# Kernel tuning notes

Measured on AMD Instinct MI355X. Metric: run time of the kernel, lower is better.

Reference implementation:

```python
import jax, jax.numpy as jnp
import numpy as np
from jax import lax

P = 4
PSIZE = P * P
ITERS = 3
EPS = 1e-8
LAMBDA = 1e-3  # inverse-temperature used by the EM routing sigmoid (yl-1993 style)
LN2PI_HALF = 0.5 * float(np.log(2.0 * np.pi))


def extract_patches(x, K, stride, pad):
    """x: (b,h,w,c) -> (b,oh,ow,K*K,c) sliding-window patches."""
    if pad:
        x = jnp.pad(x, ((0, 0), (pad, pad), (pad, pad), (0, 0)))
    b, h, w, c = x.shape
    oh = (h - K) // stride + 1
    ow = (w - K) // stride + 1
    slices = []
    for ki in range(K):
        for kj in range(K):
            slices.append(x[:, ki:ki + stride * (oh - 1) + 1:stride,
                             kj:kj + stride * (ow - 1) + 1:stride, :])
    return jnp.stack(slices, axis=3)  # (b,oh,ow,K*K,c)


def em_routing(v, a_in, beta_u, beta_a, iters=ITERS):
    """EM routing (Hinton et al. 2018).
    v: (n, Bin, Cout, PSIZE) votes, a_in: (n, Bin, 1) input activations.
    Returns mu: (n, Cout, PSIZE), a_out: (n, Cout).
    """
    n, Bin, Cout, psize = v.shape
    r = jnp.full((n, Bin, Cout), 1.0 / Cout, dtype=v.dtype)
    mu = None
    a_out = None
    for it in range(iters):
        # ---- M step ----
        r_w = r * a_in                                    # (n,Bin,Cout)
        r_sum = r_w.sum(axis=1, keepdims=True)            # (n,1,Cout)
        coeff = (r_w / (r_sum + EPS))[..., None]          # (n,Bin,Cout,1)
        mu = jnp.sum(coeff * v, axis=1, keepdims=True)    # (n,1,Cout,psize)
        sigma_sq = jnp.sum(coeff * (v - mu) ** 2, axis=1, keepdims=True) + EPS
        cost_h = (beta_u[None, None, :, None] + 0.5 * jnp.log(sigma_sq)) * r_sum[..., None]
        a_out = jax.nn.sigmoid(LAMBDA * (beta_a[None, None, :] - cost_h.sum(axis=3)))  # (n,1,Cout)
        # ---- E step ----
        if it < iters - 1:
            ln_p = -(v - mu) ** 2 / (2.0 * sigma_sq) - 0.5 * jnp.log(sigma_sq) - LN2PI_HALF
            ln_ap = ln_p.sum(axis=3) + jnp.log(EPS + a_out)  # (n,Bin,Cout)
            r = jax.nn.softmax(ln_ap, axis=2)
    return mu[:, 0], a_out[:, 0]


def depthwise_caps(pose, a, W, bu, ba, K, stride):
    """DepthWiseConvCaps: each capsule type routes its own KxK spatial patch to one
    output capsule of the same type. W: (K*K, B, P, P)."""
    b = pose.shape[0]
    Bc = a.shape[-1]
    pad = K // 2
    pp = extract_patches(pose, K, stride, pad)  # (b,oh,ow,KK,B*PSIZE)
    ap = extract_patches(a, K, stride, pad)     # (b,oh,ow,KK,B)
    oh, ow = pp.shape[1], pp.shape[2]
    pm = pp.reshape(b, oh, ow, K * K, Bc, P, P)
    v = jnp.einsum('bhwkcij,kcjl->bhwkcil', pm, W)            # (b,oh,ow,KK,B,P,P)
    v = v.transpose(0, 1, 2, 4, 3, 5, 6).reshape(b * oh * ow * Bc, K * K, 1, PSIZE)
    a_in = ap.transpose(0, 1, 2, 4, 3).reshape(b * oh * ow * Bc, K * K, 1)
    mu, a_out = em_routing(v, a_in, bu, ba)
    return mu.reshape(b, oh, ow, Bc * PSIZE), a_out.reshape(b, oh, ow, Bc)


def conv_caps_1x1(pose, a, W, bu, ba):
    """ConvCaps with K=1, stride=1: per-position routing Bin -> Cout. W: (Bin,Cout,P,P)."""
    b, h, w, _ = pose.shape
    Bc, Cc = W.shape[0], W.shape[1]
    pm = pose.reshape(b * h * w, Bc, P, P)
    v = jnp.einsum('nbij,bcjl->nbcil', pm, W).reshape(b * h * w, Bc, Cc, PSIZE)
    a_in = a.reshape(b * h * w, Bc)[..., None]
    mu, a_out = em_routing(v, a_in, bu, ba)
    return mu.reshape(b, h, w, Cc * PSIZE), a_out.reshape(b, h, w, Cc)


def class_caps(pose, a, W, bu, ba):
    """Class ConvCaps: w_shared across positions + coordinate addition. W: (D,E,P,P)."""
    b, h, w, _ = pose.shape
    D, E = W.shape[0], W.shape[1]
    pm = pose.reshape(b, h, w, D, P, P)
    v = jnp.einsum('bhwdij,dejl->bhwdeil', pm, W).reshape(b, h, w, D, E, PSIZE)
    # coordinate addition on the first two vote components
    coord = jnp.zeros((h, w, PSIZE), v.dtype)
    coord = coord.at[:, :, 0].add(jnp.arange(h, dtype=v.dtype)[:, None] / h)
    coord = coord.at[:, :, 1].add(jnp.arange(w, dtype=v.dtype)[None, :] / w)
    v = v + coord[None, :, :, None, None, :]
    v = v.reshape(b, h * w * D, E, PSIZE)
    a_in = a.reshape(b, h * w * D, 1)
    mu, a_out = em_routing(v, a_in, bu, ba)
    return mu, a_out  # (b,E,PSIZE), (b,E)


def _forward(x, conv1_w, conv1_b, prim_pose_w, prim_pose_b, prim_a_w, prim_a_b,
             dw1_w, dw1_bu, dw1_ba, cc1_w, cc1_bu, cc1_ba,
             dw2_w, dw2_bu, dw2_ba, cc2_w, cc2_bu, cc2_ba,
             cls_w, cls_bu, cls_ba):
    # conv stem: k5 s2 valid
    y = lax.conv_general_dilated(x, conv1_w, (2, 2), 'VALID',
                                 dimension_numbers=('NHWC', 'HWIO', 'NHWC'))
    y = jax.nn.relu(y + conv1_b)
    # primary caps: 1x1 convs for pose and activation
    pose = jnp.einsum('bhwc,cd->bhwd', y, prim_pose_w) + prim_pose_b   # (b,h,w,B*PSIZE)
    a = jax.nn.sigmoid(jnp.einsum('bhwc,cd->bhwd', y, prim_a_w) + prim_a_b)  # (b,h,w,B)
    pose, a = depthwise_caps(pose, a, dw1_w, dw1_bu, dw1_ba, K=7, stride=2)
    pose, a = conv_caps_1x1(pose, a, cc1_w, cc1_bu, cc1_ba)
    pose, a = depthwise_caps(pose, a, dw2_w, dw2_bu, dw2_ba, K=5, stride=2)
    pose, a = conv_caps_1x1(pose, a, cc2_w, cc2_bu, cc2_ba)
    pose_cls, a_cls = class_caps(pose, a, cls_w, cls_bu, cls_ba)
    return a_cls  # (b, E)


def setup_inputs() -> dict:
    key = jax.random.key(0)
    ks = jax.random.split(key, 10)
    f32 = jnp.float32
    d = {}
    d['x'] = jax.random.normal(ks[0], (32, 64, 64, 1), f32)
    d['conv1_w'] = jax.random.normal(ks[1], (5, 5, 1, 64), f32) * 0.1
    d['conv1_b'] = jnp.zeros((64,), f32)
    d['prim_pose_w'] = jax.random.normal(ks[2], (64, 128), f32) * 0.1
    d['prim_pose_b'] = jnp.zeros((128,), f32)
    d['prim_a_w'] = jax.random.normal(ks[3], (64, 8), f32) * 0.1
    d['prim_a_b'] = jnp.zeros((8,), f32)
    d['dw1_w'] = jax.random.normal(ks[4], (49, 8, 4, 4), f32) * 0.25
    d['dw1_bu'] = jnp.zeros((1,), f32)
    d['dw1_ba'] = jnp.zeros((1,), f32)
    d['cc1_w'] = jax.random.normal(ks[5], (8, 16, 4, 4), f32) * 0.25
    d['cc1_bu'] = jnp.zeros((16,), f32)
    d['cc1_ba'] = jnp.zeros((16,), f32)
    d['dw2_w'] = jax.random.normal(ks[6], (25, 16, 4, 4), f32) * 0.25
    d['dw2_bu'] = jnp.zeros((1,), f32)
    d['dw2_ba'] = jnp.zeros((1,), f32)
    d['cc2_w'] = jax.random.normal(ks[7], (16, 16, 4, 4), f32) * 0.25
    d['cc2_bu'] = jnp.zeros((16,), f32)
    d['cc2_ba'] = jnp.zeros((16,), f32)
    d['cls_w'] = jax.random.normal(ks[8], (16, 10, 4, 4), f32) * 0.25
    d['cls_bu'] = jnp.zeros((10,), f32)
    d['cls_ba'] = jnp.zeros((10,), f32)
    return d


def reference(x, conv1_w, conv1_b, prim_pose_w, prim_pose_b, prim_a_w, prim_a_b,
              dw1_w, dw1_bu, dw1_ba, cc1_w, cc1_bu, cc1_ba,
              dw2_w, dw2_bu, dw2_ba, cc2_w, cc2_bu, cc2_ba,
              cls_w, cls_bu, cls_ba):
    return _forward(x, conv1_w, conv1_b, prim_pose_w, prim_pose_b, prim_a_w, prim_a_b,
                    dw1_w, dw1_bu, dw1_ba, cc1_w, cc1_bu, cc1_ba,
                    dw2_w, dw2_bu, dw2_ba, cc2_w, cc2_bu, cc2_ba,
                    cls_w, cls_bu, cls_ba)
```

## Files before the change

### kernel.cpp

```cpp
#include <hip/hip_runtime.h>
#include <hip/hip_bf16.h>

#define EPS 1e-8f
#define LAMBDA 1e-3f
#define LN2PI_HALF 0.9189385332046727f

__device__ __forceinline__ float sigmoidf(float x) { return 1.f / (1.f + __expf(-x)); }

__global__ __launch_bounds__(256) void stem_primary_kernel(
    const float* __restrict__ x, const float* __restrict__ w,
    const float* __restrict__ bias,
    const float* __restrict__ wp, const float* __restrict__ bp,
    const float* __restrict__ wa, const float* __restrict__ ba,
    float* __restrict__ pose, float* __restrict__ a) {
  __shared__ __align__(16) float wc_s[25][64];
  __shared__ __align__(16) float wa_s[64][8];
  __shared__ __align__(16) float bias_s[64];
  __shared__ __align__(16) float bp_s[128];
  __shared__ float ba_s[8];
  __shared__ float xs[5][63];
  __shared__ __align__(16) float ys_u[2][15][68];

  int t = threadIdx.x;
  int oi = blockIdx.x % 30;
  int b  = blockIdx.x / 30;

  for (int q = t; q < 400;  q += 256) ((float4*)wc_s)[q] = ((const float4*)w)[q];
  for (int q = t; q < 128;  q += 256) ((float4*)wa_s)[q] = ((const float4*)wa)[q];
  if (t < 64) bias_s[t] = bias[t];
  if (t < 128) bp_s[t] = bp[t];
  if (t < 8) ba_s[t] = ba[t];
  for (int q = t; q < 315; q += 256) {
    int ki = q / 63, col = q % 63;
    xs[ki][col] = x[(b * 64 + 2 * oi + ki) * 64 + col];
  }
  __syncthreads();

  for (int q = t; q < 480; q += 256) {
    int pos = q >> 4, c4 = (q & 15) << 2;
    float4 s4 = *(const float4*)&bias_s[c4];
#pragma unroll
    for (int ki = 0; ki < 5; ++ki)
#pragma unroll
      for (int kj = 0; kj < 5; ++kj) {
        float xv = xs[ki][2 * pos + kj];
        const float4 wv = *(const float4*)&wc_s[ki * 5 + kj][c4];
        s4.x += xv * wv.x;
        s4.y += xv * wv.y;
        s4.z += xv * wv.z;
        s4.w += xv * wv.w;
      }
    s4.x = fmaxf(s4.x, 0.f);
    s4.y = fmaxf(s4.y, 0.f);
    s4.z = fmaxf(s4.z, 0.f);
    s4.w = fmaxf(s4.w, 0.f);
    *(float4*)&ys_u[pos & 1][pos >> 1][c4] = s4;
  }
  __syncthreads();

  int w_ = t >> 7, d = t & 127;
  float acc[15];
#pragma unroll
  for (int j = 0; j < 15; ++j) acc[j] = bp_s[d];
  const float* wpd = wp + d;
#pragma unroll 4
  for (int c4 = 0; c4 < 64; c4 += 4) {
    float w0 = wpd[(c4 + 0) * 128];
    float w1 = wpd[(c4 + 1) * 128];
    float w2 = wpd[(c4 + 2) * 128];
    float w3 = wpd[(c4 + 3) * 128];
#pragma unroll
    for (int j = 0; j < 15; ++j) {
      const float4 yv = *(const float4*)&ys_u[w_][j][c4];
      acc[j] += yv.x * w0 + yv.y * w1 + yv.z * w2 + yv.w * w3;
    }
  }
  size_t rowb = (size_t)(b * 30 + oi) * 30;
#pragma unroll
  for (int j = 0; j < 15; ++j)
    pose[(rowb + w_ + 2 * j) * 128 + d] = acc[j];

  if (t < 240) {
    int pos = t >> 3, jj = t & 7;
    float s = ba_s[jj];
#pragma unroll 8
    for (int c = 0; c < 64; ++c) s += ys_u[pos & 1][pos >> 1][c] * wa_s[c][jj];
    a[(rowb + pos) * 8 + jj] = sigmoidf(s);
  }
}

template <int K, int BC, int HIN, int WIN, int HOUT, int WOUT, int OIG, int NG>
__global__ __launch_bounds__(256) void dw_caps_kernel(
    const float* __restrict__ pose_in, const float* __restrict__ a_in,
    const float* __restrict__ Wt,
    const float* __restrict__ bu_p, const float* __restrict__ ba_p,
    float* __restrict__ pose_out, float* __restrict__ a_out) {
  constexpr int PAD = K / 2;
  constexpr int RA = (2 * (OIG - 1) + K < HIN) ? (2 * (OIG - 1) + K) : HIN;
  constexpr int TOT = OIG * WOUT * 16;
  constexpr int KM = (TOT + 255) / 256;
  __shared__ __align__(16) float tp[RA * WIN * 20];
  __shared__ float ta[RA * WIN];
  __shared__ __align__(16) float wt[K * K * 16];

  int t = threadIdx.x;
  int g = (NG > 1) ? (blockIdx.x % NG) : 0;
  int c = (blockIdx.x / NG) % BC;
  int b = blockIdx.x / (NG * BC);
  int oi_lo = g * OIG;
  int rlo = max(0, 2 * oi_lo - PAD);
  int rhi = min(HIN, 2 * (oi_lo + OIG - 1) - PAD + K);
  int nrows = rhi - rlo;

  for (int q = t; q < K * K * 16; q += 256) {
    int tap = q >> 4, lj = q & 15, l = lj >> 2, j = lj & 3;
    wt[tap * 16 + lj] = Wt[((size_t)tap * BC + c) * 16 + j * 4 + l];
  }
  for (int q = t; q < nrows * WIN; q += 256) {
    int row = q / WIN, col = q % WIN;
    ta[q] = a_in[((size_t)((b * HIN + rlo + row) * WIN + col)) * BC + c];
  }
  for (int q = t; q < nrows * WIN * 4; q += 256) {
    int quad = q & 3, pc = q >> 2;
    int row = pc / WIN, col = pc % WIN;
    const float4 src = *(const float4*)(pose_in +
        (((size_t)((b * HIN + rlo + row) * WIN + col)) * BC + c) * 16 + quad * 4);
    *(float4*)(tp + (row * WIN + col) * 20 + quad * 4) = src;
  }
  __syncthreads();

  const int p = t & 15;
  const int ip = p >> 2, l = p & 3;
  const float* wtl = wt + l * 4;

  int ih0[KM], iw0[KM];
  float rsum[KM], acc[KM], acc2[KM];
#pragma unroll
  for (int k = 0; k < KM; ++k) {
    int s = t + k * 256;
    int pr = s >> 4;
    int oj = pr % WOUT;
    int oi = oi_lo + pr / WOUT;
    ih0[k] = 2 * oi - PAD;
    iw0[k] = 2 * oj - PAD;
    rsum[k] = 0.f;
    acc[k] = 0.f;
    acc2[k] = 0.f;
  }

#pragma unroll 1
  for (int ki = 0; ki < K; ++ki) {
    int rb[KM];
    bool vk[KM];
#pragma unroll
    for (int k = 0; k < KM; ++k) {
      int ih = ih0[k] + ki;
      vk[k] = (t + k * 256 < TOT) && (ih >= 0) && (ih < HIN);
      rb[k] = (ih - rlo) * WIN;
    }
#pragma unroll
    for (int kj = 0; kj < K; ++kj) {
      const float4 wr = *(const float4*)(wtl + (ki * K + kj) * 16);
#pragma unroll
      for (int k = 0; k < KM; ++k) {
        if (!vk[k]) continue;
        int iw = iw0[k] + kj;
        if (iw < 0 || iw >= WIN) continue;
        int idx = rb[k] + iw;
        float ak = ta[idx];
        const float4 pm = *(const float4*)(tp + idx * 20 + ip * 4);
        float v = pm.x * wr.x + pm.y * wr.y + pm.z * wr.z + pm.w * wr.w;
        rsum[k] += ak;
        float av = ak * v;
        acc[k] += av;
        acc2[k] += av * v;
      }
    }
  }

#pragma unroll 1
  for (int k = 0; k < KM; ++k) {
    int s = t + k * 256;
    if (s >= TOT) break;
    int pr = s >> 4;
    int oj = pr % WOUT;
    int oi = oi_lo + pr / WOUT;
    float inv = 1.f / (rsum[k] + EPS);
    float mu = acc[k] * inv;
    float S = rsum[k] * inv;
    float sg = acc2[k] * inv - mu * mu * (2.f - S);
    sg = fmaxf(sg, 0.f) + EPS;
    float hl = 0.5f * __logf(sg);
    float ls = hl;
    ls += __shfl_xor(ls, 1, 64);
    ls += __shfl_xor(ls, 2, 64);
    ls += __shfl_xor(ls, 4, 64);
    ls += __shfl_xor(ls, 8, 64);

    size_t obase = ((size_t)(b * HOUT + oi) * WOUT + oj) * BC + c;
    pose_out[obase * 16 + p] = mu;
    if (p == 0) {
      float cost = rsum[k] * (16.f * bu_p[0] + ls);
      a_out[obase] = sigmoidf(LAMBDA * (ba_p[0] - cost));
    }
  }
}

template <int BIN>
__global__ __launch_bounds__(256) void cc_em_kernel(
    const float* __restrict__ pose_in, const float* __restrict__ a_arr,
    const float* __restrict__ Wt,
    const float* __restrict__ bu_p, const float* __restrict__ ba_p,
    float* __restrict__ pose_out, float* __restrict__ a_out) {
  constexpr int COUT = 16;
  __shared__ float wt_s[BIN * COUT * 20];
  int t = threadIdx.x;
  for (int idx = t; idx < BIN * COUT * 16; idx += 256) {
    int lk = idx & 15, l = lk >> 2, k = lk & 3;
    int bc = idx >> 4;
    wt_s[bc * 20 + l * 4 + k] = Wt[bc * 16 + k * 4 + l];
  }
  __syncthreads();

  int wave = t >> 6, lane = t & 63;
  int n = blockIdx.x * 4 + wave;
  int c = lane >> 2;
  int q = lane & 3;

  float ain[BIN], rw[BIN];
  float4 pmq[BIN];
#pragma unroll
  for (int b = 0; b < BIN; ++b) {
    ain[b] = a_arr[(size_t)n * BIN + b];
    rw[b] = (1.f / 16.f) * ain[b];
    pmq[b] = *(const float4*)(pose_in + (size_t)n * BIN * 16 + b * 16 + q * 4);
  }
  float bu = bu_p[c], ba = ba_p[c];

  float v[BIN][4];
#pragma unroll
  for (int b = 0; b < BIN; ++b) {
    const float* wr = wt_s + (b * 16 + c) * 20;
#pragma unroll
    for (int l = 0; l < 4; ++l) {
      const float4 w4 = *(const float4*)(wr + l * 4);
      v[b][l] = pmq[b].x * w4.x + pmq[b].y * w4.y + pmq[b].z * w4.z + pmq[b].w * w4.w;
    }
  }

  float mu[4], inv2[4], lsum = 0.f, ao = 0.f;
#pragma unroll 1
  for (int it = 0; it < 3; ++it) {
    float sA = 0.f, sV[4] = {0, 0, 0, 0}, sV2[4] = {0, 0, 0, 0};
#pragma unroll
    for (int b = 0; b < BIN; ++b) {
      sA += rw[b];
#pragma unroll
      for (int l = 0; l < 4; ++l) {
        float rv = rw[b] * v[b][l];
        sV[l] += rv;
        sV2[l] += rv * v[b][l];
      }
    }
    float inv = 1.f / (sA + EPS);
    float S = sA * inv;
    lsum = 0.f;
#pragma unroll
    for (int l = 0; l < 4; ++l) {
      mu[l] = sV[l] * inv;
      float sg = sV2[l] * inv - mu[l] * mu[l] * (2.f - S) + EPS;
      sg = fmaxf(sg, EPS);
      inv2[l] = 0.5f / sg;
      lsum += 0.5f * __logf(sg);
    }
    lsum += __shfl_xor(lsum, 1, 64);
    lsum += __shfl_xor(lsum, 2, 64);
    float cost = sA * (16.f * bu + lsum);
    ao = sigmoidf(LAMBDA * (ba - cost));

    if (it < 2) {
      float term[BIN];
#pragma unroll
      for (int b = 0; b < BIN; ++b) {
        float s = 0.f;
#pragma unroll
        for (int l = 0; l < 4; ++l) {
          float d = v[b][l] - mu[l];
          s += d * d * inv2[l];
        }
        term[b] = s;
      }
#pragma unroll
      for (int b = 0; b < BIN; ++b) {
        term[b] += __shfl_xor(term[b], 1, 64);
        term[b] += __shfl_xor(term[b], 2, 64);
      }
      float basec = __logf(EPS + ao) - lsum - 16.f * LN2PI_HALF;
      float lnap[BIN], Z[BIN];
#pragma unroll
      for (int b = 0; b < BIN; ++b) lnap[b] = basec - term[b];
      float mx[BIN];
#pragma unroll
      for (int b = 0; b < BIN; ++b) mx[b] = lnap[b];
#pragma unroll
      for (int m = 4; m < 64; m <<= 1)
#pragma unroll
        for (int b = 0; b < BIN; ++b) mx[b] = fmaxf(mx[b], __shfl_xor(mx[b], m, 64));
#pragma unroll
      for (int b = 0; b < BIN; ++b) { lnap[b] = __expf(lnap[b] - mx[b]); Z[b] = lnap[b]; }
#pragma unroll
      for (int m = 4; m < 64; m <<= 1)
#pragma unroll
        for (int b = 0; b < BIN; ++b) Z[b] += __shfl_xor(Z[b], m, 64);
#pragma unroll
      for (int b = 0; b < BIN; ++b) rw[b] = lnap[b] / Z[b] * ain[b];
    }
  }
  float4 om = make_float4(mu[0], mu[1], mu[2], mu[3]);
  *(float4*)(pose_out + (size_t)n * 256 + c * 16 + q * 4) = om;
  if (q == 0) a_out[(size_t)n * COUT + c] = ao;
}

__global__ __launch_bounds__(256) void cc_em_coop16_kernel(
    const float* __restrict__ pose_in, const float* __restrict__ a_arr,
    const float* __restrict__ Wt,
    const float* __restrict__ bu_p, const float* __restrict__ ba_p,
    float* __restrict__ pose_out, float* __restrict__ a_out) {
  __shared__ float red_s[2][4][64 * 9];
  int t = threadIdx.x;
  int w = t >> 6, lane = t & 63;
  int c = lane >> 2, q = lane & 3;
  int n = blockIdx.x;

  float ain[4], rw[4], v[4][4];
  const float* pbase = pose_in + (size_t)n * 256;
#pragma unroll
  for (int i = 0; i < 4; ++i) {
    int b = w * 4 + i;
    ain[i] = a_arr[(size_t)n * 16 + b];
    rw[i] = (1.f / 16.f) * ain[i];
    const float4 pm = *(const float4*)(pbase + b * 16 + q * 4);
    const float* wr = Wt + (b * 16 + c) * 16;
    const float4 r0 = *(const float4*)(wr + 0);
    const float4 r1 = *(const float4*)(wr + 4);
    const float4 r2 = *(const float4*)(wr + 8);
    const float4 r3 = *(const float4*)(wr + 12);
    v[i][0] = pm.x * r0.x + pm.y * r1.x + pm.z * r2.x + pm.w * r3.x;
    v[i][1] = pm.x * r0.y + pm.y * r1.y + pm.z * r2.y + pm.w * r3.y;
    v[i][2] = pm.x * r0.z + pm.y * r1.z + pm.z * r2.z + pm.w * r3.z;
    v[i][3] = pm.x * r0.w + pm.y * r1.w + pm.z * r2.w + pm.w * r3.w;
  }
  float bu = bu_p[c], ba = ba_p[c];

  float mu[4], inv2[4], lsum = 0.f, ao = 0.f;
#pragma unroll 1
  for (int it = 0; it < 3; ++it) {
    float psA = 0.f, psV[4] = {0, 0, 0, 0}, psV2[4] = {0, 0, 0, 0};
#pragma unroll
    for (int i = 0; i < 4; ++i) {
      psA += rw[i];
#pragma unroll
      for (int l = 0; l < 4; ++l) {
        float rv = rw[i] * v[i][l];
        psV[l] += rv;
        psV2[l] += rv * v[i][l];
      }
    }
    {
      float* rs = &red_s[it & 1][w][lane * 9];
      rs[0] = psA;
#pragma unroll
      for (int l = 0; l < 4; ++l) { rs[1 + l] = psV[l]; rs[5 + l] = psV2[l]; }
    }
    __syncthreads();
    float sA = 0.f, sV[4] = {0, 0, 0, 0}, sV2[4] = {0, 0, 0, 0};
#pragma unroll
    for (int w2 = 0; w2 < 4; ++w2) {
      const float* rr = &red_s[it & 1][w2][lane * 9];
      sA += rr[0];
#pragma unroll
      for (int l = 0; l < 4; ++l) { sV[l] += rr[1 + l]; sV2[l] += rr[5 + l]; }
    }
    float inv = 1.f / (sA + EPS);
    float S = sA * inv;
    lsum = 0.f;
#pragma unroll
    for (int l = 0; l < 4; ++l) {
      mu[l] = sV[l] * inv;
      float sg = sV2[l] * inv - mu[l] * mu[l] * (2.f - S) + EPS;
      sg = fmaxf(sg, EPS);
      inv2[l] = 0.5f / sg;
      lsum += 0.5f * __logf(sg);
    }
    lsum += __shfl_xor(lsum, 1, 64);
    lsum += __shfl_xor(lsum, 2, 64);
    float cost = sA * (16.f * bu + lsum);
    ao = sigmoidf(LAMBDA * (ba - cost));

    if (it < 2) {
      float term[4];
#pragma unroll
      for (int i = 0; i < 4; ++i) {
        float s = 0.f;
#pragma unroll
        for (int l = 0; l < 4; ++l) {
          float d = v[i][l] - mu[l];
          s += d * d * inv2[l];
        }
        term[i] = s;
      }
#pragma unroll
      for (int i = 0; i < 4; ++i) {
        term[i] += __shfl_xor(term[i], 1, 64);
        term[i] += __shfl_xor(term[i], 2, 64);
      }
      float basec = __logf(EPS + ao) - lsum - 16.f * LN2PI_HALF;
      float lnap[4], mx[4], Z[4];
#pragma unroll
      for (int i = 0; i < 4; ++i) { lnap[i] = basec - term[i]; mx[i] = lnap[i]; }
#pragma unroll
      for (int m = 4; m < 64; m <<= 1)
#pragma unroll
        for (int i = 0; i < 4; ++i) mx[i] = fmaxf(mx[i], __shfl_xor(mx[i], m, 64));
#pragma unroll
      for (int i = 0; i < 4; ++i) { lnap[i] = __expf(lnap[i] - mx[i]); Z[i] = lnap[i]; }
#pragma unroll
      for (int m = 4; m < 64; m <<= 1)
#pragma unroll
        for (int i = 0; i < 4; ++i) Z[i] += __shfl_xor(Z[i], m, 64);
#pragma unroll
      for (int i = 0; i < 4; ++i) rw[i] = lnap[i] / Z[i] * ain[i];
    }
  }
  if (w == 0) {
    *(float4*)(pose_out + (size_t)n * 256 + c * 16 + q * 4) =
        make_float4(mu[0], mu[1], mu[2], mu[3]);
    if (q == 0) a_out[(size_t)n * 16 + c] = ao;
  }
}

__global__ __launch_bounds__(256) void cls_m_kernel(
    const float* __restrict__ pose5, const float* __restrict__ a5,
    const float* __restrict__ X, const float* __restrict__ W,
    const float* __restrict__ bu_p, const float* __restrict__ ba_p,
    float* __restrict__ mu_g, float* __restrict__ inv2_g,
    float* __restrict__ base_g, float* __restrict__ out,
    int first, int last) {
  int blk = blockIdx.x;
  int c = blk % 10, b = blk / 10;
  int t = threadIdx.x;
  int lane = t & 63, wv = t >> 6;
  const float* pg = pose5 + (size_t)b * 16384;
  __shared__ float w_s[16][16];
  {
    int d = t & 15, jj = t >> 4;
    w_s[jj][d] = W[(d * 10 + c) * 16 + jj];
  }
  __syncthreads();
  const int d = t & 15;
  float wf[16];
#pragma unroll
  for (int jj = 0; jj < 16; ++jj) wf[jj] = w_s[jj][d];

  float sA = 0.f, sV[16], sV2[16];
#pragma unroll
  for (int p = 0; p < 16; ++p) { sV[p] = 0.f; sV2[p] = 0.f; }
#pragma unroll 1
  for (int rep = 0; rep < 4; ++rep) {
    int bi = rep * 256 + t;
    int pos = bi >> 4;
    float rw = first ? 0.1f * a5[(size_t)b * 1024 + bi]
                     : X[(size_t)blk * 1024 + bi];
    float ci = (float)(pos >> 3) * 0.125f;
    float cj = (float)(pos & 7) * 0.125f;
    const float* pp = pg + pos * 256 + d * 16;
    float pmr[16];
#pragma unroll
    for (int q = 0; q < 16; ++q) pmr[q] = pp[q];
    sA += rw;
#pragma unroll
    for (int p = 0; p < 16; ++p) {
      int ip = p >> 2, l = p & 3;
      float v = pmr[ip * 4 + 0] * wf[0 * 4 + l] + pmr[ip * 4 + 1] * wf[1 * 4 + l]
              + pmr[ip * 4 + 2] * wf[2 * 4 + l] + pmr[ip * 4 + 3] * wf[3 * 4 + l];
      if (p == 0) v += ci;
      else if (p == 1) v += cj;
      float rv = rw * v;
      sV[p] += rv;
      sV2[p] += rv * v;
    }
  }
#pragma unroll
  for (int off = 1; off < 64; off <<= 1) {
    sA += __shfl_xor(sA, off, 64);
#pragma unroll
    for (int p = 0; p < 16; ++p) {
      sV[p]  += __shfl_xor(sV[p],  off, 64);
      sV2[p] += __shfl_xor(sV2[p], off, 64);
    }
  }
  __shared__ float red[4][36];
  if (lane == 0) {
    red[wv][0] = sA;
#pragma unroll
    for (int p = 0; p < 16; ++p) { red[wv][1 + p] = sV[p]; red[wv][17 + p] = sV2[p]; }
  }
  __syncthreads();
  if (t < 16) {
    int p = t;
    float sAf  = red[0][0] + red[1][0] + red[2][0] + red[3][0];
    float sVf  = red[0][1+p] + red[1][1+p] + red[2][1+p] + red[3][1+p];
    float sV2f = red[0][17+p] + red[1][17+p] + red[2][17+p] + red[3][17+p];
    float inv = 1.f / (sAf + EPS);
    float S = sAf * inv;
    float mu = sVf * inv;
    float sg = sV2f * inv - mu * mu * (2.f - S) + EPS;
    sg = fmaxf(sg, EPS);
    mu_g[blk * 16 + p] = mu;
    inv2_g[blk * 16 + p] = 0.5f / sg;
    float hl = 0.5f * __logf(sg);
    float lsum = hl;
    lsum += __shfl_xor(lsum, 1, 64);
    lsum += __shfl_xor(lsum, 2, 64);
    lsum += __shfl_xor(lsum, 4, 64);
    lsum += __shfl_xor(lsum, 8, 64);
    if (p == 0) {
      float cost = sAf * (16.f * bu_p[c] + lsum);
      float ao = sigmoidf(LAMBDA * (ba_p[c] - cost));
      base_g[blk] = __logf(EPS + ao) - lsum - 16.f * LN2PI_HALF;
      if (last) out[blk] = ao;
    }
  }
}

__global__ __launch_bounds__(256) void cls_e_kernel(
    const float* __restrict__ pose5, const float* __restrict__ a5,
    const float* __restrict__ W,
    const float* __restrict__ mu_g, const float* __restrict__ inv2_g,
    const float* __restrict__ base_g, float* __restrict__ X) {
  int b = blockIdx.x >> 2;
  int t = threadIdx.x;
  int bi = ((blockIdx.x & 3) << 8) + t;
  const float* pg = pose5 + (size_t)b * 16384;
  __shared__ float w2[10][16][16];
  __shared__ float mu_s[160];
  __shared__ float inv2_s[160];
  __shared__ float base_s[10];
  for (int q = t; q < 2560; q += 256) {
    int dd = q & 15, jj = (q >> 4) & 15, c = q >> 8;
    w2[c][jj][dd] = W[(dd * 10 + c) * 16 + jj];
  }
  if (t < 160) { mu_s[t] = mu_g[b * 160 + t]; inv2_s[t] = inv2_g[b * 160 + t]; }
  if (t >= 160 && t < 170) base_s[t - 160] = base_g[b * 10 + (t - 160)];
  __syncthreads();

  int pos = bi >> 4, d2 = bi & 15;
  float ci = (float)(pos >> 3) * 0.125f;
  float cj = (float)(pos & 7) * 0.125f;
  const float* pp = pg + pos * 256 + d2 * 16;
  float pmr[16];
#pragma unroll
  for (int q = 0; q < 16; ++q) pmr[q] = pp[q];
  float lnap[10];
#pragma unroll 1
  for (int c = 0; c < 10; ++c) {
    float wf[16];
#pragma unroll
    for (int jj = 0; jj < 16; ++jj) wf[jj] = w2[c][jj][d2];
    float s = base_s[c];
#pragma unroll
    for (int p = 0; p < 16; ++p) {
      int ip = p >> 2, l = p & 3;
      float v = pmr[ip * 4 + 0] * wf[0 * 4 + l] + pmr[ip * 4 + 1] * wf[1 * 4 + l]
              + pmr[ip * 4 + 2] * wf[2 * 4 + l] + pmr[ip * 4 + 3] * wf[3 * 4 + l];
      if (p == 0) v += ci;
      else if (p == 1) v += cj;
      float dd = v - mu_s[c * 16 + p];
      s -= dd * dd * inv2_s[c * 16 + p];
    }
    lnap[c] = s;
  }
  float m = -1e30f;
#pragma unroll
  for (int c = 0; c < 10; ++c) m = fmaxf(m, lnap[c]);
  float Z = 0.f;
  float ex[10];
#pragma unroll
  for (int c = 0; c < 10; ++c) { ex[c] = __expf(lnap[c] - m); Z += ex[c]; }
  float invZ = a5[(size_t)b * 1024 + bi] / Z;
#pragma unroll
  for (int c = 0; c < 10; ++c) X[((size_t)(b * 10 + c)) * 1024 + bi] = ex[c] * invZ;
}

extern "C" void kernel_launch(void* const* d_in, const int* in_sizes, int n_in,
                              void* d_out, int out_size, void* d_ws, size_t ws_size,
                              hipStream_t stream) {
  const float* x       = (const float*)d_in[0];
  const float* conv1_w = (const float*)d_in[1];
  const float* conv1_b = (const float*)d_in[2];
  const float* pp_w    = (const float*)d_in[3];
  const float* pp_b    = (const float*)d_in[4];
  const float* pa_w    = (const float*)d_in[5];
  const float* pa_b    = (const float*)d_in[6];
  const float* dw1_w   = (const float*)d_in[7];
  const float* dw1_bu  = (const float*)d_in[8];
  const float* dw1_ba  = (const float*)d_in[9];
  const float* cc1_w   = (const float*)d_in[10];
  const float* cc1_bu  = (const float*)d_in[11];
  const float* cc1_ba  = (const float*)d_in[12];
  const float* dw2_w   = (const float*)d_in[13];
  const float* dw2_bu  = (const float*)d_in[14];
  const float* dw2_ba  = (const float*)d_in[15];
  const float* cc2_w   = (const float*)d_in[16];
  const float* cc2_bu  = (const float*)d_in[17];
  const float* cc2_ba  = (const float*)d_in[18];
  const float* cls_w   = (const float*)d_in[19];
  const float* cls_bu  = (const float*)d_in[20];
  const float* cls_ba  = (const float*)d_in[21];
  float* out = (float*)d_out;

  float* ws = (float*)d_ws;
  float* pose1 = ws;
  float* a1    = ws + 3686400;
  float* pose2 = ws + 3916800;
  float* a2    = ws + 4838400;
  float* pose3 = ws;
  float* a3    = ws + 1843200;
  float* pose4 = ws + 1958400;
  float* a4    = ws + 2482688;
  float* pose5 = ws + 2515456;
  float* a5    = ws + 3039744;
  float* Xbuf  = ws + 3072512;
  float* mu_g  = ws + 3400192;
  float* inv2_g= ws + 3405312;
  float* base_g= ws + 3410432;

  stem_primary_kernel<<<960, 256, 0, stream>>>(x, conv1_w, conv1_b,
                                               pp_w, pp_b, pa_w, pa_b, pose1, a1);
  dw_caps_kernel<7, 8, 30, 30, 15, 15, 3, 5><<<1280, 256, 0, stream>>>(
      pose1, a1, dw1_w, dw1_bu, dw1_ba, pose2, a2);
  cc_em_kernel<8><<<1800, 256, 0, stream>>>(pose2, a2, cc1_w, cc1_bu, cc1_ba, pose3, a3);
  dw_caps_kernel<5, 16, 15, 15, 8, 8, 2, 4><<<2048, 256, 0, stream>>>(
      pose3, a3, dw2_w, dw2_bu, dw2_ba, pose4, a4);
  cc_em_coop16_kernel<<<2048, 256, 0, stream>>>(pose4, a4, cc2_w, cc2_bu, cc2_ba,
                                                pose5, a5);
  cls_m_kernel<<<320, 256, 0, stream>>>(pose5, a5, Xbuf, cls_w, cls_bu, cls_ba,
                                        mu_g, inv2_g, base_g, out, 1, 0);
  cls_e_kernel<<<128, 256, 0, stream>>>(pose5, a5, cls_w, mu_g, inv2_g, base_g, Xbuf);
  cls_m_kernel<<<320, 256, 0, stream>>>(pose5, a5, Xbuf, cls_w, cls_bu, cls_ba,
                                        mu_g, inv2_g, base_g, out, 0, 0);
  cls_e_kernel<<<128, 256, 0, stream>>>(pose5, a5, cls_w, mu_g, inv2_g, base_g, Xbuf);
  cls_m_kernel<<<320, 256, 0, stream>>>(pose5, a5, Xbuf, cls_w, cls_bu, cls_ba,
                                        mu_g, inv2_g, base_g, out, 0, 1);
}
```

Baseline: 247.2 us.

## Fuse class-capsule EM routing iterations into one per-batch kernel

```diff
diff --git a/kernel.cpp b/kernel.cpp
--- a/kernel.cpp
+++ b/kernel.cpp
@@ -439,157 +439,147 @@
   }
 }
 
-__global__ __launch_bounds__(256) void cls_m_kernel(
-    const float* __restrict__ pose5, const float* __restrict__ a5,
-    const float* __restrict__ X, const float* __restrict__ W,
-    const float* __restrict__ bu_p, const float* __restrict__ ba_p,
-    float* __restrict__ mu_g, float* __restrict__ inv2_g,
-    float* __restrict__ base_g, float* __restrict__ out,
-    int first, int last) {
-  int blk = blockIdx.x;
-  int c = blk % 10, b = blk / 10;
-  int t = threadIdx.x;
-  int lane = t & 63, wv = t >> 6;
-  const float* pg = pose5 + (size_t)b * 16384;
-  __shared__ float w_s[16][16];
-  {
-    int d = t & 15, jj = t >> 4;
-    w_s[jj][d] = W[(d * 10 + c) * 16 + jj];
-  }
-  __syncthreads();
-  const int d = t & 15;
-  float wf[16];
-#pragma unroll
-  for (int jj = 0; jj < 16; ++jj) wf[jj] = w_s[jj][d];
-
-  float sA = 0.f, sV[16], sV2[16];
-#pragma unroll
-  for (int p = 0; p < 16; ++p) { sV[p] = 0.f; sV2[p] = 0.f; }
-#pragma unroll 1
-  for (int rep = 0; rep < 4; ++rep) {
-    int bi = rep * 256 + t;
-    int pos = bi >> 4;
-    float rw = first ? 0.1f * a5[(size_t)b * 1024 + bi]
-                     : X[(size_t)blk * 1024 + bi];
-    float ci = (float)(pos >> 3) * 0.125f;
-    float cj = (float)(pos & 7) * 0.125f;
-    const float* pp = pg + pos * 256 + d * 16;
-    float pmr[16];
-#pragma unroll
-    for (int q = 0; q < 16; ++q) pmr[q] = pp[q];
-    sA += rw;
-#pragma unroll
-    for (int p = 0; p < 16; ++p) {
-      int ip = p >> 2, l = p & 3;
-      float v = pmr[ip * 4 + 0] * wf[0 * 4 + l] + pmr[ip * 4 + 1] * wf[1 * 4 + l]
-              + pmr[ip * 4 + 2] * wf[2 * 4 + l] + pmr[ip * 4 + 3] * wf[3 * 4 + l];
-      if (p == 0) v += ci;
-      else if (p == 1) v += cj;
-      float rv = rw * v;
-      sV[p] += rv;
-      sV2[p] += rv * v;
-    }
-  }
-#pragma unroll
-  for (int off = 1; off < 64; off <<= 1) {
-    sA += __shfl_xor(sA, off, 64);
-#pragma unroll
-    for (int p = 0; p < 16; ++p) {
-      sV[p]  += __shfl_xor(sV[p],  off, 64);
-      sV2[p] += __shfl_xor(sV2[p], off, 64);
-    }
-  }
-  __shared__ float red[4][36];
-  if (lane == 0) {
-    red[wv][0] = sA;
-#pragma unroll
-    for (int p = 0; p < 16; ++p) { red[wv][1 + p] = sV[p]; red[wv][17 + p] = sV2[p]; }
-  }
-  __syncthreads();
-  if (t < 16) {
-    int p = t;
-    float sAf  = red[0][0] + red[1][0] + red[2][0] + red[3][0];
-    float sVf  = red[0][1+p] + red[1][1+p] + red[2][1+p] + red[3][1+p];
-    float sV2f = red[0][17+p] + red[1][17+p] + red[2][17+p] + red[3][17+p];
-    float inv = 1.f / (sAf + EPS);
-    float S = sAf * inv;
-    float mu = sVf * inv;
-    float sg = sV2f * inv - mu * mu * (2.f - S) + EPS;
-    sg = fmaxf(sg, EPS);
-    mu_g[blk * 16 + p] = mu;
-    inv2_g[blk * 16 + p] = 0.5f / sg;
-    float hl = 0.5f * __logf(sg);
-    float lsum = hl;
-    lsum += __shfl_xor(lsum, 1, 64);
-    lsum += __shfl_xor(lsum, 2, 64);
-    lsum += __shfl_xor(lsum, 4, 64);
-    lsum += __shfl_xor(lsum, 8, 64);
-    if (p == 0) {
-      float cost = sAf * (16.f * bu_p[c] + lsum);
-      float ao = sigmoidf(LAMBDA * (ba_p[c] - cost));
-      base_g[blk] = __logf(EPS + ao) - lsum - 16.f * LN2PI_HALF;
-      if (last) out[blk] = ao;
-    }
-  }
-}
-
-__global__ __launch_bounds__(256) void cls_e_kernel(
+__global__ __launch_bounds__(1024) void cls_fused_kernel(
     const float* __restrict__ pose5, const float* __restrict__ a5,
     const float* __restrict__ W,
-    const float* __restrict__ mu_g, const float* __restrict__ inv2_g,
-    const float* __restrict__ base_g, float* __restrict__ X) {
-  int b = blockIdx.x >> 2;
+    const float* __restrict__ bu_p, const float* __restrict__ ba_p,
+    float* __restrict__ out) {
+  int b = blockIdx.x;
   int t = threadIdx.x;
-  int bi = ((blockIdx.x & 3) << 8) + t;
-  const float* pg = pose5 + (size_t)b * 16384;
+  int pos = t >> 4, d = t & 15;
+  int wv = t >> 6, lane = t & 63;
+
   __shared__ float w2[10][16][16];
-  __shared__ float mu_s[160];
-  __shared__ float inv2_s[160];
+  __shared__ float red[16][10][33];
+  __shared__ float fin[10][33];
+  __shared__ float mu_s[10][16];
+  __shared__ float inv2_s[10][16];
   __shared__ float base_s[10];
-  for (int q = t; q < 2560; q += 256) {
+
+  for (int q = t; q < 2560; q += 1024) {
     int dd = q & 15, jj = (q >> 4) & 15, c = q >> 8;
     w2[c][jj][dd] = W[(dd * 10 + c) * 16 + jj];
   }
-  if (t < 160) { mu_s[t] = mu_g[b * 160 + t]; inv2_s[t] = inv2_g[b * 160 + t]; }
-  if (t >= 160 && t < 170) base_s[t - 160] = base_g[b * 10 + (t - 160)];
-  __syncthreads();
-
-  int pos = bi >> 4, d2 = bi & 15;
+
+  float pmr[16];
+  const float* pp = pose5 + (size_t)b * 16384 + pos * 256 + d * 16;
+#pragma unroll
+  for (int q = 0; q < 16; ++q) pmr[q] = pp[q];
+  float ain = a5[(size_t)b * 1024 + t];
   float ci = (float)(pos >> 3) * 0.125f;
   float cj = (float)(pos & 7) * 0.125f;
-  const float* pp = pg + pos * 256 + d2 * 16;
-  float pmr[16];
-#pragma unroll
-  for (int q = 0; q < 16; ++q) pmr[q] = pp[q];
-  float lnap[10];
+
+  float X_reg[10];
+#pragma unroll
+  for (int c = 0; c < 10; ++c) X_reg[c] = 0.1f * ain;
+
+  __syncthreads();
+
 #pragma unroll 1
-  for (int c = 0; c < 10; ++c) {
-    float wf[16];
-#pragma unroll
-    for (int jj = 0; jj < 16; ++jj) wf[jj] = w2[c][jj][d2];
-    float s = base_s[c];
-#pragma unroll
-    for (int p = 0; p < 16; ++p) {
-      int ip = p >> 2, l = p & 3;
-      float v = pmr[ip * 4 + 0] * wf[0 * 4 + l] + pmr[ip * 4 + 1] * wf[1 * 4 + l]
-              + pmr[ip * 4 + 2] * wf[2 * 4 + l] + pmr[ip * 4 + 3] * wf[3 * 4 + l];
-      if (p == 0) v += ci;
-      else if (p == 1) v += cj;
-      float dd = v - mu_s[c * 16 + p];
-      s -= dd * dd * inv2_s[c * 16 + p];
-    }
-    lnap[c] = s;
-  }
-  float m = -1e30f;
-#pragma unroll
-  for (int c = 0; c < 10; ++c) m = fmaxf(m, lnap[c]);
-  float Z = 0.f;
-  float ex[10];
-#pragma unroll
-  for (int c = 0; c < 10; ++c) { ex[c] = __expf(lnap[c] - m); Z += ex[c]; }
-  float invZ = a5[(size_t)b * 1024 + bi] / Z;
-#pragma unroll
-  for (int c = 0; c < 10; ++c) X[((size_t)(b * 10 + c)) * 1024 + bi] = ex[c] * invZ;
+  for (int it = 0; it < 3; ++it) {
+#pragma unroll 1
+    for (int c = 0; c < 10; ++c) {
+      float wf[16];
+#pragma unroll
+      for (int jj = 0; jj < 16; ++jj) wf[jj] = w2[c][jj][d];
+      float rw = X_reg[c];
+      float sA = rw, sV[16], sV2[16];
+#pragma unroll
+      for (int p = 0; p < 16; ++p) {
+        int ip = p >> 2, l = p & 3;
+        float v = pmr[ip * 4 + 0] * wf[0 * 4 + l] + pmr[ip * 4 + 1] * wf[1 * 4 + l]
+                + pmr[ip * 4 + 2] * wf[2 * 4 + l] + pmr[ip * 4 + 3] * wf[3 * 4 + l];
+        if (p == 0) v += ci;
+        else if (p == 1) v += cj;
+        float rv = rw * v;
+        sV[p] = rv;
+        sV2[p] = rv * v;
+      }
+#pragma unroll
+      for (int off = 1; off < 64; off <<= 1) {
+        sA += __shfl_xor(sA, off, 64);
+#pragma unroll
+        for (int p = 0; p < 16; ++p) {
+          sV[p]  += __shfl_xor(sV[p],  off, 64);
+          sV2[p] += __shfl_xor(sV2[p], off, 64);
+        }
+      }
+      if (lane == 0) {
+        red[wv][c][0] = sA;
+#pragma unroll
+        for (int p = 0; p < 16; ++p) {
+          red[wv][c][1 + p]  = sV[p];
+          red[wv][c][17 + p] = sV2[p];
+        }
+      }
+    }
+    __syncthreads();
+    if (t < 330) {
+      int c = t / 33, vq = t % 33;
+      float s = 0.f;
+#pragma unroll
+      for (int w = 0; w < 16; ++w) s += red[w][c][vq];
+      fin[c][vq] = s;
+    }
+    __syncthreads();
+    if (t < 160) {
+      int c = t >> 4, p = t & 15;
+      float sAf  = fin[c][0];
+      float sVf  = fin[c][1 + p];
+      float sV2f = fin[c][17 + p];
+      float inv = 1.f / (sAf + EPS);
+      float S = sAf * inv;
+      float mu = sVf * inv;
+      float sg = sV2f * inv - mu * mu * (2.f - S) + EPS;
+      sg = fmaxf(sg, EPS);
+      mu_s[c][p] = mu;
+      inv2_s[c][p] = 0.5f / sg;
+      float hl = 0.5f * __logf(sg);
+      float lsum = hl;
+      lsum += __shfl_xor(lsum, 1, 64);
+      lsum += __shfl_xor(lsum, 2, 64);
+      lsum += __shfl_xor(lsum, 4, 64);
+      lsum += __shfl_xor(lsum, 8, 64);
+      if (p == 0) {
+        float cost = sAf * (16.f * bu_p[c] + lsum);
+        float ao = sigmoidf(LAMBDA * (ba_p[c] - cost));
+        base_s[c] = __logf(EPS + ao) - lsum - 16.f * LN2PI_HALF;
+        if (it == 2) out[b * 10 + c] = ao;
+      }
+    }
+    __syncthreads();
+    if (it < 2) {
+      float lnap[10];
+#pragma unroll 1
+      for (int c = 0; c < 10; ++c) {
+        float wf[16];
+#pragma unroll
+        for (int jj = 0; jj < 16; ++jj) wf[jj] = w2[c][jj][d];
+        float s = base_s[c];
+#pragma unroll
+        for (int p = 0; p < 16; ++p) {
+          int ip = p >> 2, l = p & 3;
+          float v = pmr[ip * 4 + 0] * wf[0 * 4 + l] + pmr[ip * 4 + 1] * wf[1 * 4 + l]
+                  + pmr[ip * 4 + 2] * wf[2 * 4 + l] + pmr[ip * 4 + 3] * wf[3 * 4 + l];
+          if (p == 0) v += ci;
+          else if (p == 1) v += cj;
+          float dd2 = v - mu_s[c][p];
+          s -= dd2 * dd2 * inv2_s[c][p];
+        }
+        lnap[c] = s;
+      }
+      float m = -1e30f;
+#pragma unroll
+      for (int c = 0; c < 10; ++c) m = fmaxf(m, lnap[c]);
+      float Z = 0.f;
+      float ex[10];
+#pragma unroll
+      for (int c = 0; c < 10; ++c) { ex[c] = __expf(lnap[c] - m); Z += ex[c]; }
+      float invZ = ain / Z;
+#pragma unroll
+      for (int c = 0; c < 10; ++c) X_reg[c] = ex[c] * invZ;
+    }
+  }
 }
 
 extern "C" void kernel_launch(void* const* d_in, const int* in_sizes, int n_in,
@@ -630,10 +620,6 @@
   float* a4    = ws + 2482688;
   float* pose5 = ws + 2515456;
   float* a5    = ws + 3039744;
-  float* Xbuf  = ws + 3072512;
-  float* mu_g  = ws + 3400192;
-  float* inv2_g= ws + 3405312;
-  float* base_g= ws + 3410432;
 
   stem_primary_kernel<<<960, 256, 0, stream>>>(x, conv1_w, conv1_b,
                                                pp_w, pp_b, pa_w, pa_b, pose1, a1);
@@ -644,12 +630,5 @@
       pose3, a3, dw2_w, dw2_bu, dw2_ba, pose4, a4);
   cc_em_coop16_kernel<<<2048, 256, 0, stream>>>(pose4, a4, cc2_w, cc2_bu, cc2_ba,
                                                 pose5, a5);
-  cls_m_kernel<<<320, 256, 0, stream>>>(pose5, a5, Xbuf, cls_w, cls_bu, cls_ba,
-                                        mu_g, inv2_g, base_g, out, 1, 0);
-  cls_e_kernel<<<128, 256, 0, stream>>>(pose5, a5, cls_w, mu_g, inv2_g, base_g, Xbuf);
-  cls_m_kernel<<<320, 256, 0, stream>>>(pose5, a5, Xbuf, cls_w, cls_bu, cls_ba,
-                                        mu_g, inv2_g, base_g, out, 0, 0);
-  cls_e_kernel<<<128, 256, 0, stream>>>(pose5, a5, cls_w, mu_g, inv2_g, base_g, Xbuf);
-  cls_m_kernel<<<320, 256, 0, stream>>>(pose5, a5, Xbuf, cls_w, cls_bu, cls_ba,
-                                        mu_g, inv2_g, base_g, out, 0, 1);
+  cls_fused_kernel<<<32, 1024, 0, stream>>>(pose5, a5, cls_w, cls_bu, cls_ba, out);
 }
```

New measurement: 532.8 us. 2.15x slower.

## Split cc1 EM routing across two waves per position with LDS reduction

Applied to the files above, without the earlier changes.

```diff
diff --git a/kernel.cpp b/kernel.cpp
--- a/kernel.cpp
+++ b/kernel.cpp
@@ -206,61 +206,66 @@
   }
 }
 
-template <int BIN>
-__global__ __launch_bounds__(256) void cc_em_kernel(
+__global__ __launch_bounds__(256) void cc_em_coop8_kernel(
     const float* __restrict__ pose_in, const float* __restrict__ a_arr,
     const float* __restrict__ Wt,
     const float* __restrict__ bu_p, const float* __restrict__ ba_p,
     float* __restrict__ pose_out, float* __restrict__ a_out) {
-  constexpr int COUT = 16;
-  __shared__ float wt_s[BIN * COUT * 20];
+  __shared__ float red_s[2][2][2][64 * 9];
   int t = threadIdx.x;
-  for (int idx = t; idx < BIN * COUT * 16; idx += 256) {
-    int lk = idx & 15, l = lk >> 2, k = lk & 3;
-    int bc = idx >> 4;
-    wt_s[bc * 20 + l * 4 + k] = Wt[bc * 16 + k * 4 + l];
-  }
-  __syncthreads();
-
-  int wave = t >> 6, lane = t & 63;
-  int n = blockIdx.x * 4 + wave;
-  int c = lane >> 2;
-  int q = lane & 3;
-
-  float ain[BIN], rw[BIN];
-  float4 pmq[BIN];
-#pragma unroll
-  for (int b = 0; b < BIN; ++b) {
-    ain[b] = a_arr[(size_t)n * BIN + b];
-    rw[b] = (1.f / 16.f) * ain[b];
-    pmq[b] = *(const float4*)(pose_in + (size_t)n * BIN * 16 + b * 16 + q * 4);
+  int w = t >> 6, lane = t & 63;
+  int prob = w >> 1, wh = w & 1;
+  int c = lane >> 2, q = lane & 3;
+  int n = blockIdx.x * 2 + prob;
+
+  float ain[4], rw[4], v[4][4];
+  const float* pbase = pose_in + (size_t)n * 128;
+#pragma unroll
+  for (int i = 0; i < 4; ++i) {
+    int b = wh * 4 + i;
+    ain[i] = a_arr[(size_t)n * 8 + b];
+    rw[i] = (1.f / 16.f) * ain[i];
+    const float4 pm = *(const float4*)(pbase + b * 16 + q * 4);
+    const float* wr = Wt + (b * 16 + c) * 16;
+    const float4 r0 = *(const float4*)(wr + 0);
+    const float4 r1 = *(const float4*)(wr + 4);
+    const float4 r2 = *(const float4*)(wr + 8);
+    const float4 r3 = *(const float4*)(wr + 12);
+    v[i][0] = pm.x * r0.x + pm.y * r1.x + pm.z * r2.x + pm.w * r3.x;
+    v[i][1] = pm.x * r0.y + pm.y * r1.y + pm.z * r2.y + pm.w * r3.y;
+    v[i][2] = pm.x * r0.z + pm.y * r1.z + pm.z * r2.z + pm.w * r3.z;
+    v[i][3] = pm.x * r0.w + pm.y * r1.w + pm.z * r2.w + pm.w * r3.w;
   }
   float bu = bu_p[c], ba = ba_p[c];
-
-  float v[BIN][4];
-#pragma unroll
-  for (int b = 0; b < BIN; ++b) {
-    const float* wr = wt_s + (b * 16 + c) * 20;
-#pragma unroll
-    for (int l = 0; l < 4; ++l) {
-      const float4 w4 = *(const float4*)(wr + l * 4);
-      v[b][l] = pmq[b].x * w4.x + pmq[b].y * w4.y + pmq[b].z * w4.z + pmq[b].w * w4.w;
-    }
-  }
 
   float mu[4], inv2[4], lsum = 0.f, ao = 0.f;
 #pragma unroll 1
   for (int it = 0; it < 3; ++it) {
+    float psA = 0.f, psV[4] = {0, 0, 0, 0}, psV2[4] = {0, 0, 0, 0};
+#pragma unroll
+    for (int i = 0; i < 4; ++i) {
+      psA += rw[i];
+#pragma unroll
+      for (int l = 0; l < 4; ++l) {
+        float rv = rw[i] * v[i][l];
+        psV[l] += rv;
+        psV2[l] += rv * v[i][l];
+      }
+    }
+    {
+      float* rs = &red_s[it & 1][prob][wh][lane * 9];
+      rs[0] = psA;
+#pragma unroll
+      for (int l = 0; l < 4; ++l) { rs[1 + l] = psV[l]; rs[5 + l] = psV2[l]; }
+    }
+    __syncthreads();
     float sA = 0.f, sV[4] = {0, 0, 0, 0}, sV2[4] = {0, 0, 0, 0};
 #pragma unroll
-    for (int b = 0; b < BIN; ++b) {
-      sA += rw[b];
-#pragma unroll
-      for (int l = 0; l < 4; ++l) {
-        float rv = rw[b] * v[b][l];
-        sV[l] += rv;
-        sV2[l] += rv * v[b][l];
-      }
+    for (int w2 = 0; w2 < 2; ++w2) {
+      const float* rr = &red_s[it & 1][prob][w2][lane * 9];
+      sA += rr[0];
+#pragma unroll
+      for (int l = 0; l < 4; ++l) { sV[l] += rr[1 + l]; sV2[l] += rr[5 + l]; }
     }
     float inv = 1.f / (sA + EPS);
     float S = sA * inv;
@@ -279,46 +284,45 @@
     ao = sigmoidf(LAMBDA * (ba - cost));
 
     if (it < 2) {
-      float term[BIN];
-#pragma unroll
-      for (int b = 0; b < BIN; ++b) {
+      float term[4];
+#pragma unroll
+      for (int i = 0; i < 4; ++i) {
         float s = 0.f;
 #pragma unroll
         for (int l = 0; l < 4; ++l) {
-          float d = v[b][l] - mu[l];
+          float d = v[i][l] - mu[l];
           s += d * d * inv2[l];
         }
-        term[b] = s;
-      }
-#pragma unroll
-      for (int b = 0; b < BIN; ++b) {
-        term[b] += __shfl_xor(term[b], 1, 64);
-        term[b] += __shfl_xor(term[b], 2, 64);
+        term[i] = s;
+      }
+#pragma unroll
+      for (int i = 0; i < 4; ++i) {
+        term[i] += __shfl_xor(term[i], 1, 64);
+        term[i] += __shfl_xor(term[i], 2, 64);
       }
       float basec = __logf(EPS + ao) - lsum - 16.f * LN2PI_HALF;
-      float lnap[BIN], Z[BIN];
-#pragma unroll
-      for (int b = 0; b < BIN; ++b) lnap[b] = basec - term[b];
-      float mx[BIN];
-#pragma unroll
-      for (int b = 0; b < BIN; ++b) mx[b] = lnap[b];
+      float lnap[4], mx[4], Z[4];
+#pragma unroll
+      for (int i = 0; i < 4; ++i) { lnap[i] = basec - term[i]; mx[i] = lnap[i]; }
 #pragma unroll
       for (int m = 4; m < 64; m <<= 1)
 #pragma unroll
-        for (int b = 0; b < BIN; ++b) mx[b] = fmaxf(mx[b], __shfl_xor(mx[b], m, 64));
-#pragma unroll
-      for (int b = 0; b < BIN; ++b) { lnap[b] = __expf(lnap[b] - mx[b]); Z[b] = lnap[b]; }
+        for (int i = 0; i < 4; ++i) mx[i] = fmaxf(mx[i], __shfl_xor(mx[i], m, 64));
+#pragma unroll
+      for (int i = 0; i < 4; ++i) { lnap[i] = __expf(lnap[i] - mx[i]); Z[i] = lnap[i]; }
 #pragma unroll
       for (int m = 4; m < 64; m <<= 1)
 #pragma unroll
-        for (int b = 0; b < BIN; ++b) Z[b] += __shfl_xor(Z[b], m, 64);
-#pragma unroll
-      for (int b = 0; b < BIN; ++b) rw[b] = lnap[b] / Z[b] * ain[b];
-    }
-  }
-  float4 om = make_float4(mu[0], mu[1], mu[2], mu[3]);
-  *(float4*)(pose_out + (size_t)n * 256 + c * 16 + q * 4) = om;
-  if (q == 0) a_out[(size_t)n * COUT + c] = ao;
+        for (int i = 0; i < 4; ++i) Z[i] += __shfl_xor(Z[i], m, 64);
+#pragma unroll
+      for (int i = 0; i < 4; ++i) rw[i] = lnap[i] / Z[i] * ain[i];
+    }
+  }
+  if (wh == 0) {
+    *(float4*)(pose_out + (size_t)n * 256 + c * 16 + q * 4) =
+        make_float4(mu[0], mu[1], mu[2], mu[3]);
+    if (q == 0) a_out[(size_t)n * 16 + c] = ao;
+  }
 }
 
 __global__ __launch_bounds__(256) void cc_em_coop16_kernel(
@@ -639,7 +643,8 @@
                                                pp_w, pp_b, pa_w, pa_b, pose1, a1);
   dw_caps_kernel<7, 8, 30, 30, 15, 15, 3, 5><<<1280, 256, 0, stream>>>(
       pose1, a1, dw1_w, dw1_bu, dw1_ba, pose2, a2);
-  cc_em_kernel<8><<<1800, 256, 0, stream>>>(pose2, a2, cc1_w, cc1_bu, cc1_ba, pose3, a3);
+  cc_em_coop8_kernel<<<3600, 256, 0, stream>>>(pose2, a2, cc1_w, cc1_bu, cc1_ba,
+                                               pose3, a3);
   dw_caps_kernel<5, 16, 15, 15, 8, 8, 2, 4><<<2048, 256, 0, stream>>>(
       pose3, a3, dw2_w, dw2_bu, dw2_ba, pose4, a4);
   cc_em_coop16_kernel<<<2048, 256, 0, stream>>>(pose4, a4, cc2_w, cc2_bu, cc2_ba,
```

Result: no change. 250.3 us (median of 3 runs) (+1.2%).
